# Optimization experiments

Measured on AMD Instinct MI355X. Metric: run time of the kernel, lower is better.

## Reference

```python
import jax, jax.numpy as jnp
import numpy as np

IN_FEATURES = 1024
OUT_FEATURES = 1024
NUM_EXPERTS = 4
RANK = 16  # total_rank=64 / num_experts=4, rem=0 -> equal ranks
NETWORK_ALPHA = 64.0


def setup_inputs() -> dict:
    key = jax.random.key(0)
    k1, k2, k3, k4 = jax.random.split(key, 4)
    hidden_states = jax.random.normal(k1, (4, 4096, IN_FEATURES), dtype=jnp.float32)
    alpha = jax.random.uniform(k2, (4, NUM_EXPERTS), dtype=jnp.float32)
    # down: K Linear(in, r) weights, each [r, in], init std=1/r (as in torch init)
    down_w = jax.random.normal(k3, (NUM_EXPERTS, RANK, IN_FEATURES), dtype=jnp.float32) / RANK
    # up: K Linear(r, out) weights, each [out, r]. Torch inits these to zero,
    # which would make the output identically zero; use small random values so
    # the reference exercises the full math.
    up_w = jax.random.normal(k4, (NUM_EXPERTS, OUT_FEATURES, RANK), dtype=jnp.float32) * 0.02
    return {"hidden_states": hidden_states, "alpha": alpha, "down_w": down_w, "up_w": up_w}


def reference(hidden_states, alpha, down_w, up_w):
    # hidden_states: [B, N, D]; alpha: [B, K]
    # down_w: [K, r, D]; up_w: [K, out, r]
    scale = NETWORK_ALPHA / RANK  # network_alpha / rank_per_expert (equal ranks)
    # per-expert down projection: [B, K, N, r]
    low = jnp.einsum('bnd,krd->bknr', hidden_states, down_w)
    # up projection + scale + alpha-weighted sum over experts, fused: [B, N, out]
    out = jnp.einsum('bknr,kor,bk->bno', low, up_w, alpha) * scale
    return out
```

## Files before the change

### kernel.cpp

```cpp
#include <hip/hip_runtime.h>

namespace {

typedef short  bf16x8 __attribute__((ext_vector_type(8)));
typedef float  f32x4  __attribute__((ext_vector_type(4)));

constexpr int D = 1024;
constexpr int O = 1024;

__device__ __forceinline__ short f2bf(float f) {
    unsigned u = __builtin_bit_cast(unsigned, f);
    u += 0x7fffu + ((u >> 16) & 1u);
    return (short)(u >> 16);
}

__device__ __forceinline__ bf16x8 cvt8(const float4 a, const float4 b) {
    bf16x8 v;
    v[0] = f2bf(a.x); v[1] = f2bf(a.y); v[2] = f2bf(a.z); v[3] = f2bf(a.w);
    v[4] = f2bf(b.x); v[5] = f2bf(b.y); v[6] = f2bf(b.z); v[7] = f2bf(b.w);
    return v;
}

__global__ void __launch_bounds__(512) lora_mfma_k(
        const float* __restrict__ hs,
        const float* __restrict__ alpha,
        const float* __restrict__ dw,
        const float* __restrict__ uw,
        float* __restrict__ out) {
    __shared__ __align__(16) short bs[18432];
    __shared__ __align__(16) short lowb[4][16][72];
    __shared__ float pacc[4][16][64];

    const int t    = threadIdx.x;
    const int w    = t >> 6;
    const int lane = t & 63;
    const int rt   = w >> 1;
    const int kh   = w & 1;
    const int fr   = lane & 15;
    const int kgi  = lane >> 4;
    const int kg   = kgi * 8;
    const int rowblk = blockIdx.x * 64;
    const int b      = rowblk >> 12;
    const int myrow  = rowblk + rt * 16 + fr;

    f32x4 acc[4];
#pragma unroll
    for (int nt = 0; nt < 4; ++nt) acc[nt] = (f32x4){0.f, 0.f, 0.f, 0.f};

#pragma unroll 1
    for (int c = 0; c < 4; ++c) {
        __syncthreads();
#pragma unroll
        for (int i = 0; i < 4; ++i) {
            const int e  = i * 512 + t;
            const int kr = e >> 5;
            const int cc = e & 31;
            const float* sp = dw + (size_t)kr * D + c * 256 + cc * 8;
            const float4 s0 = *reinterpret_cast<const float4*>(sp);
            const float4 s1 = *reinterpret_cast<const float4*>(sp + 4);
            *reinterpret_cast<bf16x8*>(&bs[kr * 264 + cc * 8]) = cvt8(s0, s1);
        }
        __syncthreads();

        const float* ap = hs + (size_t)myrow * D + c * 256 + kh * 128 + kg;
#pragma unroll
        for (int ks = 0; ks < 4; ++ks) {
            const float4 a0 = *reinterpret_cast<const float4*>(ap + ks * 32);
            const float4 a1 = *reinterpret_cast<const float4*>(ap + ks * 32 + 4);
            const bf16x8 av = cvt8(a0, a1);
#pragma unroll
            for (int nt = 0; nt < 4; ++nt) {
                const bf16x8 bv = *reinterpret_cast<const bf16x8*>(
                    &bs[(nt * 16 + fr) * 264 + kh * 128 + ks * 32 + kg]);
                acc[nt] = __builtin_amdgcn_mfma_f32_16x16x32_bf16(av, bv, acc[nt], 0, 0, 0);
            }
        }
    }

    __syncthreads();
    if (kh) {
#pragma unroll
        for (int nt = 0; nt < 4; ++nt)
#pragma unroll
            for (int j = 0; j < 4; ++j)
                pacc[rt][nt * 4 + j][lane] = acc[nt][j];
    }
    __syncthreads();
    if (!kh) {
#pragma unroll
        for (int nt = 0; nt < 4; ++nt) {
            const float sc = alpha[b * 4 + nt] * 4.0f;
#pragma unroll
            for (int j = 0; j < 4; ++j) {
                const float v = (acc[nt][j] + pacc[rt][nt * 4 + j][lane]) * sc;
                lowb[rt][kgi * 4 + j][nt * 16 + fr] = f2bf(v);
            }
        }
    }
    __syncthreads();

    const bf16x8 pa0 = *reinterpret_cast<const bf16x8*>(&lowb[rt][fr][kg]);
    const bf16x8 pa1 = *reinterpret_cast<const bf16x8*>(&lowb[rt][fr][32 + kg]);

    float* op = out + (size_t)(rowblk + rt * 16 + kgi * 4) * O;

#pragma unroll 1
    for (int oc = 0; oc < 4; ++oc) {
        __syncthreads();
#pragma unroll
        for (int i = 0; i < 4; ++i) {
            const int e  = i * 512 + t;
            const int o  = e >> 3;
            const int cc = e & 7;
            const int k  = cc >> 1;
            const int r0 = (cc & 1) * 8;
            const float* sp = uw + (size_t)k * 16384 + (size_t)(oc * 256 + o) * 16 + r0;
            const float4 s0 = *reinterpret_cast<const float4*>(sp);
            const float4 s1 = *reinterpret_cast<const float4*>(sp + 4);
            *reinterpret_cast<bf16x8*>(&bs[o * 72 + cc * 8]) = cvt8(s0, s1);
        }
        __syncthreads();

#pragma unroll
        for (int ntl = 0; ntl < 8; ++ntl) {
            const int nt = kh * 8 + ntl;
            const bf16x8 b0 = *reinterpret_cast<const bf16x8*>(&bs[(nt * 16 + fr) * 72 + kg]);
            const bf16x8 b1 = *reinterpret_cast<const bf16x8*>(&bs[(nt * 16 + fr) * 72 + 32 + kg]);
            f32x4 c2 = (f32x4){0.f, 0.f, 0.f, 0.f};
            c2 = __builtin_amdgcn_mfma_f32_16x16x32_bf16(pa0, b0, c2, 0, 0, 0);
            c2 = __builtin_amdgcn_mfma_f32_16x16x32_bf16(pa1, b1, c2, 0, 0, 0);
#pragma unroll
            for (int j = 0; j < 4; ++j)
                op[(size_t)j * O + oc * 256 + nt * 16 + fr] = c2[j];
        }
    }
}

}

extern "C" void kernel_launch(void* const* d_in, const int* in_sizes, int n_in,
                              void* d_out, int out_size, void* d_ws, size_t ws_size,
                              hipStream_t stream) {
    const float* hs    = (const float*)d_in[0];
    const float* alpha = (const float*)d_in[1];
    const float* dw    = (const float*)d_in[2];
    const float* uw    = (const float*)d_in[3];
    float* outp = (float*)d_out;

    hipLaunchKernelGGL(lora_mfma_k, dim3(256), dim3(512), 0, stream,
                       hs, alpha, dw, uw, outp);
}
```

Baseline: 38.83 us.

## Double-buffer weight staging in LDS to overlap weight loads with MFMA compute

Splits the shared weight buffer into two stages. The next chunk of down or up weights is loaded into registers before computing on the current stage, then converted and written to the other buffer. The first up-projection chunk is prefetched during the last down-projection chunk. This removes one barrier per iteration and hides global weight-load latency behind the MFMA work, at the cost of twice the weight LDS footprint and more live registers.

```diff
diff --git a/kernel.cpp b/kernel.cpp
--- a/kernel.cpp
+++ b/kernel.cpp
@@ -21,13 +21,86 @@
     return v;
 }
 
+struct StageRegs { float4 a[4]; float4 b[4]; };
+
+__device__ __forceinline__ void issue_dw(const float* __restrict__ dw, int c, int t,
+                                         StageRegs& r) {
+#pragma unroll
+    for (int i = 0; i < 4; ++i) {
+        const int e = i * 512 + t, kr = e >> 5, cc = e & 31;
+        const float* sp = dw + (size_t)kr * D + c * 256 + cc * 8;
+        r.a[i] = *reinterpret_cast<const float4*>(sp);
+        r.b[i] = *reinterpret_cast<const float4*>(sp + 4);
+    }
+}
+__device__ __forceinline__ void write_p1(short* buf, int t, const StageRegs& r) {
+#pragma unroll
+    for (int i = 0; i < 4; ++i) {
+        const int e = i * 512 + t, kr = e >> 5, cc = e & 31;
+        *reinterpret_cast<bf16x8*>(&buf[kr * 264 + cc * 8]) = cvt8(r.a[i], r.b[i]);
+    }
+}
+__device__ __forceinline__ void issue_uw(const float* __restrict__ uw, int oc, int t,
+                                         StageRegs& r) {
+#pragma unroll
+    for (int i = 0; i < 4; ++i) {
+        const int e = i * 512 + t, o = e >> 3, cc = e & 7;
+        const int k = cc >> 1, r0 = (cc & 1) * 8;
+        const float* sp = uw + (size_t)k * 16384 + (size_t)(oc * 256 + o) * 16 + r0;
+        r.a[i] = *reinterpret_cast<const float4*>(sp);
+        r.b[i] = *reinterpret_cast<const float4*>(sp + 4);
+    }
+}
+__device__ __forceinline__ void write_p2(short* buf, int t, const StageRegs& r) {
+#pragma unroll
+    for (int i = 0; i < 4; ++i) {
+        const int e = i * 512 + t, o = e >> 3, cc = e & 7;
+        *reinterpret_cast<bf16x8*>(&buf[o * 72 + cc * 8]) = cvt8(r.a[i], r.b[i]);
+    }
+}
+
+__device__ __forceinline__ void compute_p1(const short* __restrict__ buf,
+                                           const float* __restrict__ ap,
+                                           int fr, int kh, int kg, f32x4* acc) {
+#pragma unroll
+    for (int ks = 0; ks < 4; ++ks) {
+        const float4 a0 = *reinterpret_cast<const float4*>(ap + ks * 32);
+        const float4 a1 = *reinterpret_cast<const float4*>(ap + ks * 32 + 4);
+        const bf16x8 av = cvt8(a0, a1);
+#pragma unroll
+        for (int nt = 0; nt < 4; ++nt) {
+            const bf16x8 bv = *reinterpret_cast<const bf16x8*>(
+                &buf[(nt * 16 + fr) * 264 + kh * 128 + ks * 32 + kg]);
+            acc[nt] = __builtin_amdgcn_mfma_f32_16x16x32_bf16(av, bv, acc[nt], 0, 0, 0);
+        }
+    }
+}
+
+__device__ __forceinline__ void compute_p2(const short* __restrict__ buf,
+                                           const bf16x8 pa0, const bf16x8 pa1,
+                                           float* __restrict__ op,
+                                           int oc, int fr, int kg, int kh) {
+#pragma unroll
+    for (int ntl = 0; ntl < 8; ++ntl) {
+        const int nt = kh * 8 + ntl;
+        const bf16x8 b0 = *reinterpret_cast<const bf16x8*>(&buf[(nt * 16 + fr) * 72 + kg]);
+        const bf16x8 b1 = *reinterpret_cast<const bf16x8*>(&buf[(nt * 16 + fr) * 72 + 32 + kg]);
+        f32x4 c2 = (f32x4){0.f, 0.f, 0.f, 0.f};
+        c2 = __builtin_amdgcn_mfma_f32_16x16x32_bf16(pa0, b0, c2, 0, 0, 0);
+        c2 = __builtin_amdgcn_mfma_f32_16x16x32_bf16(pa1, b1, c2, 0, 0, 0);
+#pragma unroll
+        for (int j = 0; j < 4; ++j)
+            op[(size_t)j * O + oc * 256 + nt * 16 + fr] = c2[j];
+    }
+}
+
 __global__ void __launch_bounds__(512) lora_mfma_k(
         const float* __restrict__ hs,
         const float* __restrict__ alpha,
         const float* __restrict__ dw,
         const float* __restrict__ uw,
         float* __restrict__ out) {
-    __shared__ __align__(16) short bs[18432];
+    __shared__ __align__(16) short bs[2][18432];
     __shared__ __align__(16) short lowb[4][16][72];
     __shared__ float pacc[4][16][64];
 
@@ -42,42 +115,29 @@
     const int rowblk = blockIdx.x * 64;
     const int b      = rowblk >> 12;
     const int myrow  = rowblk + rt * 16 + fr;
+    const float* apb = hs + (size_t)myrow * D + kh * 128 + kg;
 
+    StageRegs rg;
     f32x4 acc[4];
 #pragma unroll
     for (int nt = 0; nt < 4; ++nt) acc[nt] = (f32x4){0.f, 0.f, 0.f, 0.f};
 
-#pragma unroll 1
-    for (int c = 0; c < 4; ++c) {
+    issue_dw(dw, 0, t, rg);
+    write_p1(&bs[0][0], t, rg);
+    __syncthreads();
+
+#pragma unroll
+    for (int c = 0; c < 3; ++c) {
+        issue_dw(dw, c + 1, t, rg);
+        compute_p1(&bs[c & 1][0], apb + c * 256, fr, kh, kg, acc);
+        write_p1(&bs[(c + 1) & 1][0], t, rg);
         __syncthreads();
-#pragma unroll
-        for (int i = 0; i < 4; ++i) {
-            const int e  = i * 512 + t;
-            const int kr = e >> 5;
-            const int cc = e & 31;
-            const float* sp = dw + (size_t)kr * D + c * 256 + cc * 8;
-            const float4 s0 = *reinterpret_cast<const float4*>(sp);
-            const float4 s1 = *reinterpret_cast<const float4*>(sp + 4);
-            *reinterpret_cast<bf16x8*>(&bs[kr * 264 + cc * 8]) = cvt8(s0, s1);
-        }
-        __syncthreads();
+    }
+    issue_uw(uw, 0, t, rg);
+    compute_p1(&bs[1][0], apb + 3 * 256, fr, kh, kg, acc);
+    write_p2(&bs[0][0], t, rg);
+    __syncthreads();
 
-        const float* ap = hs + (size_t)myrow * D + c * 256 + kh * 128 + kg;
-#pragma unroll
-        for (int ks = 0; ks < 4; ++ks) {
-            const float4 a0 = *reinterpret_cast<const float4*>(ap + ks * 32);
-            const float4 a1 = *reinterpret_cast<const float4*>(ap + ks * 32 + 4);
-            const bf16x8 av = cvt8(a0, a1);
-#pragma unroll
-            for (int nt = 0; nt < 4; ++nt) {
-                const bf16x8 bv = *reinterpret_cast<const bf16x8*>(
-                    &bs[(nt * 16 + fr) * 264 + kh * 128 + ks * 32 + kg]);
-                acc[nt] = __builtin_amdgcn_mfma_f32_16x16x32_bf16(av, bv, acc[nt], 0, 0, 0);
-            }
-        }
-    }
-
-    __syncthreads();
     if (kh) {
 #pragma unroll
         for (int nt = 0; nt < 4; ++nt)
@@ -101,39 +161,16 @@
 
     const bf16x8 pa0 = *reinterpret_cast<const bf16x8*>(&lowb[rt][fr][kg]);
     const bf16x8 pa1 = *reinterpret_cast<const bf16x8*>(&lowb[rt][fr][32 + kg]);
-
     float* op = out + (size_t)(rowblk + rt * 16 + kgi * 4) * O;
 
-#pragma unroll 1
-    for (int oc = 0; oc < 4; ++oc) {
+#pragma unroll
+    for (int oc = 0; oc < 3; ++oc) {
+        issue_uw(uw, oc + 1, t, rg);
+        compute_p2(&bs[oc & 1][0], pa0, pa1, op, oc, fr, kg, kh);
+        write_p2(&bs[(oc + 1) & 1][0], t, rg);
         __syncthreads();
-#pragma unroll
-        for (int i = 0; i < 4; ++i) {
-            const int e  = i * 512 + t;
-            const int o  = e >> 3;
-            const int cc = e & 7;
-            const int k  = cc >> 1;
-            const int r0 = (cc & 1) * 8;
-            const float* sp = uw + (size_t)k * 16384 + (size_t)(oc * 256 + o) * 16 + r0;
-            const float4 s0 = *reinterpret_cast<const float4*>(sp);
-            const float4 s1 = *reinterpret_cast<const float4*>(sp + 4);
-            *reinterpret_cast<bf16x8*>(&bs[o * 72 + cc * 8]) = cvt8(s0, s1);
-        }
-        __syncthreads();
-
-#pragma unroll
-        for (int ntl = 0; ntl < 8; ++ntl) {
-            const int nt = kh * 8 + ntl;
-            const bf16x8 b0 = *reinterpret_cast<const bf16x8*>(&bs[(nt * 16 + fr) * 72 + kg]);
-            const bf16x8 b1 = *reinterpret_cast<const bf16x8*>(&bs[(nt * 16 + fr) * 72 + 32 + kg]);
-            f32x4 c2 = (f32x4){0.f, 0.f, 0.f, 0.f};
-            c2 = __builtin_amdgcn_mfma_f32_16x16x32_bf16(pa0, b0, c2, 0, 0, 0);
-            c2 = __builtin_amdgcn_mfma_f32_16x16x32_bf16(pa1, b1, c2, 0, 0, 0);
-#pragma unroll
-            for (int j = 0; j < 4; ++j)
-                op[(size_t)j * O + oc * 256 + nt * 16 + fr] = c2[j];
-        }
     }
+    compute_p2(&bs[1][0], pa0, pa1, op, 3, fr, kg, kh);
 }
 
 }
```

Result: faster. 32.60 us (-16.0%).

## Split warps into producer/consumer stages with register-resident weights

Applied to the files above, without the earlier changes.

Half the warps now compute the down projection on 16-row slices while the other half compute the up projection for the previous slice, in a 5-step software pipeline. Down and up weights are loaded once per wave into registers as bf16 instead of being staged through shared memory in chunks. This targets shared-memory staging, the many barriers, and the serialization between the two GEMM phases. In exchange it uses heavy register pressure (32 bf16x8 per thread), which may cause spills or lower occupancy, and each producer wave now reads a full K-quarter of weights.

```diff
diff --git a/kernel.cpp b/kernel.cpp
--- a/kernel.cpp
+++ b/kernel.cpp
@@ -21,118 +21,106 @@
     return v;
 }
 
-__global__ void __launch_bounds__(512) lora_mfma_k(
+__global__ void __launch_bounds__(512) lora_pc_k(
         const float* __restrict__ hs,
         const float* __restrict__ alpha,
         const float* __restrict__ dw,
         const float* __restrict__ uw,
         float* __restrict__ out) {
-    __shared__ __align__(16) short bs[18432];
-    __shared__ __align__(16) short lowb[4][16][72];
     __shared__ float pacc[4][16][64];
+    __shared__ __align__(16) short lowb[16][72];
 
     const int t    = threadIdx.x;
     const int w    = t >> 6;
     const int lane = t & 63;
-    const int rt   = w >> 1;
-    const int kh   = w & 1;
     const int fr   = lane & 15;
     const int kgi  = lane >> 4;
     const int kg   = kgi * 8;
+    const bool p1w = (w < 4);
+    const int wq   = w & 3;
     const int rowblk = blockIdx.x * 64;
     const int b      = rowblk >> 12;
-    const int myrow  = rowblk + rt * 16 + fr;
 
-    f32x4 acc[4];
+    bf16x8 regw[32];
+    if (p1w) {
 #pragma unroll
-    for (int nt = 0; nt < 4; ++nt) acc[nt] = (f32x4){0.f, 0.f, 0.f, 0.f};
+        for (int nt = 0; nt < 4; ++nt)
+#pragma unroll
+            for (int ks = 0; ks < 8; ++ks) {
+                const float* sp = dw + (size_t)(nt * 16 + fr) * D + wq * 256 + ks * 32 + kg;
+                regw[nt * 8 + ks] = cvt8(*reinterpret_cast<const float4*>(sp),
+                                         *reinterpret_cast<const float4*>(sp + 4));
+            }
+    } else {
+#pragma unroll
+        for (int nt2 = 0; nt2 < 16; ++nt2)
+#pragma unroll
+            for (int h = 0; h < 2; ++h) {
+                const int kr0 = h * 32 + kg;
+                const int k   = kr0 >> 4;
+                const int r0  = kr0 & 15;
+                const float* sp = uw + (size_t)k * 16384
+                                     + (size_t)(wq * 256 + nt2 * 16 + fr) * 16 + r0;
+                regw[nt2 * 2 + h] = cvt8(*reinterpret_cast<const float4*>(sp),
+                                         *reinterpret_cast<const float4*>(sp + 4));
+            }
+    }
+    const float sc_comb = alpha[b * 4 + ((t >> 6) & 3)] * 4.0f;
+
+    const float* apb = hs + (size_t)(rowblk + fr) * D + wq * 256 + kg;
 
 #pragma unroll 1
-    for (int c = 0; c < 4; ++c) {
-        __syncthreads();
+    for (int i = 0; i < 5; ++i) {
+        if (p1w) {
+            if (i < 4) {
+                f32x4 acc[4];
 #pragma unroll
-        for (int i = 0; i < 4; ++i) {
-            const int e  = i * 512 + t;
-            const int kr = e >> 5;
-            const int cc = e & 31;
-            const float* sp = dw + (size_t)kr * D + c * 256 + cc * 8;
-            const float4 s0 = *reinterpret_cast<const float4*>(sp);
-            const float4 s1 = *reinterpret_cast<const float4*>(sp + 4);
-            *reinterpret_cast<bf16x8*>(&bs[kr * 264 + cc * 8]) = cvt8(s0, s1);
+                for (int nt = 0; nt < 4; ++nt) acc[nt] = (f32x4){0.f, 0.f, 0.f, 0.f};
+                const float* ap = apb + (size_t)(i * 16) * D;
+#pragma unroll
+                for (int ks = 0; ks < 8; ++ks) {
+                    const float4 a0 = *reinterpret_cast<const float4*>(ap + ks * 32);
+                    const float4 a1 = *reinterpret_cast<const float4*>(ap + ks * 32 + 4);
+                    const bf16x8 av = cvt8(a0, a1);
+#pragma unroll
+                    for (int nt = 0; nt < 4; ++nt)
+                        acc[nt] = __builtin_amdgcn_mfma_f32_16x16x32_bf16(
+                            av, regw[nt * 8 + ks], acc[nt], 0, 0, 0);
+                }
+#pragma unroll
+                for (int nt = 0; nt < 4; ++nt)
+#pragma unroll
+                    for (int j = 0; j < 4; ++j)
+                        pacc[wq][nt * 4 + j][lane] = acc[nt][j];
+            }
+        } else {
+            if (i > 0) {
+                const bf16x8 pa0 = *reinterpret_cast<const bf16x8*>(&lowb[fr][kg]);
+                const bf16x8 pa1 = *reinterpret_cast<const bf16x8*>(&lowb[fr][32 + kg]);
+                float* op = out + (size_t)(rowblk + (i - 1) * 16 + kgi * 4) * O + wq * 256;
+#pragma unroll
+                for (int nt2 = 0; nt2 < 16; ++nt2) {
+                    f32x4 c2 = (f32x4){0.f, 0.f, 0.f, 0.f};
+                    c2 = __builtin_amdgcn_mfma_f32_16x16x32_bf16(pa0, regw[nt2 * 2],     c2, 0, 0, 0);
+                    c2 = __builtin_amdgcn_mfma_f32_16x16x32_bf16(pa1, regw[nt2 * 2 + 1], c2, 0, 0, 0);
+#pragma unroll
+                    for (int j = 0; j < 4; ++j)
+                        op[(size_t)j * O + nt2 * 16 + fr] = c2[j];
+                }
+            }
         }
         __syncthreads();
 
-        const float* ap = hs + (size_t)myrow * D + c * 256 + kh * 128 + kg;
+        if (p1w && i < 4) {
 #pragma unroll
-        for (int ks = 0; ks < 4; ++ks) {
-            const float4 a0 = *reinterpret_cast<const float4*>(ap + ks * 32);
-            const float4 a1 = *reinterpret_cast<const float4*>(ap + ks * 32 + 4);
-            const bf16x8 av = cvt8(a0, a1);
-#pragma unroll
-            for (int nt = 0; nt < 4; ++nt) {
-                const bf16x8 bv = *reinterpret_cast<const bf16x8*>(
-                    &bs[(nt * 16 + fr) * 264 + kh * 128 + ks * 32 + kg]);
-                acc[nt] = __builtin_amdgcn_mfma_f32_16x16x32_bf16(av, bv, acc[nt], 0, 0, 0);
+            for (int j = 0; j < 4; ++j) {
+                const int e = wq * 4 + j;
+                const float s = pacc[0][e][lane] + pacc[1][e][lane]
+                              + pacc[2][e][lane] + pacc[3][e][lane];
+                lowb[(lane >> 4) * 4 + j][wq * 16 + (lane & 15)] = f2bf(s * sc_comb);
             }
         }
-    }
-
-    __syncthreads();
-    if (kh) {
-#pragma unroll
-        for (int nt = 0; nt < 4; ++nt)
-#pragma unroll
-            for (int j = 0; j < 4; ++j)
-                pacc[rt][nt * 4 + j][lane] = acc[nt][j];
-    }
-    __syncthreads();
-    if (!kh) {
-#pragma unroll
-        for (int nt = 0; nt < 4; ++nt) {
-            const float sc = alpha[b * 4 + nt] * 4.0f;
-#pragma unroll
-            for (int j = 0; j < 4; ++j) {
-                const float v = (acc[nt][j] + pacc[rt][nt * 4 + j][lane]) * sc;
-                lowb[rt][kgi * 4 + j][nt * 16 + fr] = f2bf(v);
-            }
-        }
-    }
-    __syncthreads();
-
-    const bf16x8 pa0 = *reinterpret_cast<const bf16x8*>(&lowb[rt][fr][kg]);
-    const bf16x8 pa1 = *reinterpret_cast<const bf16x8*>(&lowb[rt][fr][32 + kg]);
-
-    float* op = out + (size_t)(rowblk + rt * 16 + kgi * 4) * O;
-
-#pragma unroll 1
-    for (int oc = 0; oc < 4; ++oc) {
         __syncthreads();
-#pragma unroll
-        for (int i = 0; i < 4; ++i) {
-            const int e  = i * 512 + t;
-            const int o  = e >> 3;
-            const int cc = e & 7;
-            const int k  = cc >> 1;
-            const int r0 = (cc & 1) * 8;
-            const float* sp = uw + (size_t)k * 16384 + (size_t)(oc * 256 + o) * 16 + r0;
-            const float4 s0 = *reinterpret_cast<const float4*>(sp);
-            const float4 s1 = *reinterpret_cast<const float4*>(sp + 4);
-            *reinterpret_cast<bf16x8*>(&bs[o * 72 + cc * 8]) = cvt8(s0, s1);
-        }
-        __syncthreads();
-
-#pragma unroll
-        for (int ntl = 0; ntl < 8; ++ntl) {
-            const int nt = kh * 8 + ntl;
-            const bf16x8 b0 = *reinterpret_cast<const bf16x8*>(&bs[(nt * 16 + fr) * 72 + kg]);
-            const bf16x8 b1 = *reinterpret_cast<const bf16x8*>(&bs[(nt * 16 + fr) * 72 + 32 + kg]);
-            f32x4 c2 = (f32x4){0.f, 0.f, 0.f, 0.f};
-            c2 = __builtin_amdgcn_mfma_f32_16x16x32_bf16(pa0, b0, c2, 0, 0, 0);
-            c2 = __builtin_amdgcn_mfma_f32_16x16x32_bf16(pa1, b1, c2, 0, 0, 0);
-#pragma unroll
-            for (int j = 0; j < 4; ++j)
-                op[(size_t)j * O + oc * 256 + nt * 16 + fr] = c2[j];
-        }
     }
 }
 
@@ -147,6 +135,6 @@
     const float* uw    = (const float*)d_in[3];
     float* outp = (float*)d_out;
 
-    hipLaunchKernelGGL(lora_mfma_k, dim3(256), dim3(512), 0, stream,
+    hipLaunchKernelGGL(lora_pc_k, dim3(256), dim3(512), 0, stream,
                        hs, alpha, dw, uw, outp);
 }
```

New measurement: 41.21 us. +6.1%, slower.
